# Kernel tuning notes

Measured on AMD Instinct MI355X. Metric: run time of the kernel, lower is better.

Reference implementation:

```python
import jax, jax.numpy as jnp
import numpy as np

COMMITMENT_COST = 0.25


def setup_inputs() -> dict:
    key = jax.random.key(0)
    k1, k2 = jax.random.split(key)
    B, D, H, W = 16, 256, 64, 64   # channel-first latents, D == embedding_dim
    K = 1024                        # num_embeddings
    z = jax.random.normal(k1, (B, D, H, W), dtype=jnp.float32)
    emb = jax.random.normal(k2, (K, D), dtype=jnp.float32)
    emb = emb / jnp.linalg.norm(emb, axis=1, keepdims=True)  # F.normalize(p=2, dim=1)
    return {"z": z, "embeddings": emb}


def reference(z, embeddings):
    D = embeddings.shape[1]
    input_shape = z.shape
    flat_z = z.reshape(-1, D)  # matches torch .view(-1, embedding_dim) on contiguous tensor
    dist = (jnp.sum(flat_z * flat_z, axis=1, keepdims=True)
            + jnp.sum(embeddings * embeddings, axis=1)
            - 2.0 * flat_z @ embeddings.T)
    encoding_indices = jnp.argmin(dist, axis=1)                       # [N]
    # one-hot @ embeddings == gather (same math, no [N,K] one-hot materialized)
    quantized = embeddings[encoding_indices].reshape(input_shape)
    e_latent_loss = jnp.mean((jax.lax.stop_gradient(quantized) - z) ** 2)
    q_latent_loss = jnp.mean((quantized - jax.lax.stop_gradient(z)) ** 2)
    vq_loss = q_latent_loss + COMMITMENT_COST * e_latent_loss
    quantized_st = z + jax.lax.stop_gradient(quantized - z)  # straight-through
    encoding_indices = encoding_indices.reshape((input_shape[0],) + input_shape[2:])
    return quantized_st, vq_loss, encoding_indices
```

## Files before the change

kernel.cpp:

```cpp
#include <hip/hip_runtime.h>
#include <stdint.h>


typedef __attribute__((ext_vector_type(8))) short short8;
typedef __attribute__((ext_vector_type(16))) float f32x16;

#define THR_S 1e-3f

__device__ __forceinline__ unsigned short f2bf(float f) {
    const unsigned int x = __float_as_uint(f);
    return (unsigned short)((x + 0x7FFFu + ((x >> 16) & 1u)) >> 16);
}
__device__ __forceinline__ float bf2f(unsigned short h) {
    return __uint_as_float(((unsigned int)h) << 16);
}

#define MFMA32(A, B, C) __builtin_amdgcn_mfma_f32_32x32x16_bf16(A, B, C, 0, 0, 0)

__global__ __launch_bounds__(256)
void eprep_kernel(const float* __restrict__ emb, unsigned short* __restrict__ eh_t,
                  unsigned short* __restrict__ el_t, float* __restrict__ enorm,
                  int* __restrict__ wlcnt) {
    const int code = blockIdx.x;
    const int k = threadIdx.x;
    if (code == 0 && k == 0) wlcnt[0] = 0;
    const float v = emb[code * 256 + k];
    const unsigned short h = f2bf(v);
    const int idx = ((k >> 4) << 14) + (code << 4) + (((k >> 3) & 1) << 3) + (k & 7);
    eh_t[idx] = h;
    el_t[idx] = f2bf(v - bf2f(h));
    float s = v * v;
#pragma unroll
    for (int o = 32; o > 0; o >>= 1) s += __shfl_xor(s, o);
    __shared__ float red[4];
    if ((k & 63) == 0) red[k >> 6] = s;
    __syncthreads();
    if (k == 0) enorm[code] = (red[0] + red[1]) + (red[2] + red[3]);
}

#define UPD(S, C, B1, I1, B2) { \
    const bool lt_ = (S) < B1; \
    B2 = lt_ ? B1 : fminf(B2, (S)); \
    I1 = lt_ ? (C) : I1; \
    B1 = lt_ ? (S) : B1; }

#define MERGE32(B1, I1, B2) { \
    const float ob1_ = __shfl_xor(B1, 32); \
    const int   oi1_ = __shfl_xor(I1, 32); \
    const float ob2_ = __shfl_xor(B2, 32); \
    const float nb2_ = fminf(fminf(B2, ob2_), fmaxf(B1, ob1_)); \
    if (ob1_ < B1 || (ob1_ == B1 && oi1_ < I1)) { B1 = ob1_; I1 = oi1_; } \
    B2 = nb2_; }

#define PFLOAD(S, U) { \
    const int un_ = (U) & 63; \
    const int ofs_ = ((un_ & 15) << 15) + ((un_ >> 4) << 10); \
    pf##S##h = *reinterpret_cast<const short8*>(ehp + ofs_); \
    pf##S##l = *reinterpret_cast<const short8*>(elp + ofs_); }

#define UNIT(S, KS) { \
    const int ko_ = (((KS) << 5) + (hi << 4)) ^ rsw; \
    const short8 bh0 = *reinterpret_cast<const short8*>(zbuf + rb0 + ko_); \
    const short8 bl0 = *reinterpret_cast<const short8*>(zbuf + 32768 + rb0 + ko_); \
    const short8 bh1 = *reinterpret_cast<const short8*>(zbuf + rb1 + ko_); \
    const short8 bl1 = *reinterpret_cast<const short8*>(zbuf + 32768 + rb1 + ko_); \
    acc1a = MFMA32(pf##S##h, bh0, acc1a); \
    acc1b = MFMA32(pf##S##h, bh1, acc1b); \
    acc2a = MFMA32(pf##S##h, bl0, acc2a); \
    acc2b = MFMA32(pf##S##h, bl1, acc2b); \
    acc2a = MFMA32(pf##S##l, bh0, acc2a); \
    acc2b = MFMA32(pf##S##l, bh1, acc2b); }

__global__ __launch_bounds__(512, 2)
void argmin_kernel(const float* __restrict__ z, const unsigned short* __restrict__ eh_t,
                   float* __restrict__ idx_out, int* __restrict__ wl,
                   int* __restrict__ wlcnt) {
    __shared__ char zbuf[65536];
    __shared__ float m_b1[8][64];
    __shared__ int   m_i1[8][64];
    __shared__ float m_b2[8][64];

    const int t = threadIdx.x;
    const int l = t & 63;
    const int w = t >> 6;
    const int cl = l & 31;
    const int hi = l >> 5;

    const float* zblk = z + (size_t)blockIdx.x * 16384;

#pragma unroll
    for (int i = 0; i < 8; ++i) {
        const int idx = i * 2048 + t * 4;
        const int row = idx >> 8, k = idx & 255;
        const float4 v = *reinterpret_cast<const float4*>(zblk + idx);
        ushort4 hv, lv;
        hv.x = f2bf(v.x); lv.x = f2bf(v.x - bf2f(hv.x));
        hv.y = f2bf(v.y); lv.y = f2bf(v.y - bf2f(hv.y));
        hv.z = f2bf(v.z); lv.z = f2bf(v.z - bf2f(hv.z));
        hv.w = f2bf(v.w); lv.w = f2bf(v.w - bf2f(hv.w));
        const int boff = row * 512 + ((k << 1) ^ ((row & 7) << 4));
        *reinterpret_cast<ushort4*>(zbuf + boff) = hv;
        *reinterpret_cast<ushort4*>(zbuf + 32768 + boff) = lv;
    }
    __syncthreads();

    const char* ehp = (const char*)eh_t + (w * 128 + cl) * 32 + hi * 16;
    const char* elp = ehp + 524288;

    const int rb0 = cl * 512;
    const int rb1 = rb0 + 16384;
    const int rsw = (cl & 7) << 4;

    f32x16 acc1a, acc2a, acc1b, acc2b;
#pragma unroll
    for (int j = 0; j < 16; ++j) { acc1a[j] = 0.f; acc2a[j] = 0.f; acc1b[j] = 0.f; acc2b[j] = 0.f; }

    float b1a = 3.4e38f, b2a = 3.4e38f, b1b = 3.4e38f, b2b = 3.4e38f;
    int   i1a = 0, i1b = 0;

    short8 pf0h, pf0l, pf1h, pf1l, pf2h, pf2l, pf3h, pf3l;
    PFLOAD(0, 0) PFLOAD(1, 1) PFLOAD(2, 2) PFLOAD(3, 3)

#pragma unroll 1
    for (int ct = 0; ct < 4; ++ct) {
#pragma unroll 1
        for (int j = 0; j < 4; ++j) {
            const int u0 = (ct << 4) + (j << 2);
            UNIT(0, ((j << 2) + 0)) PFLOAD(0, u0 + 4)
            UNIT(1, ((j << 2) + 1)) PFLOAD(1, u0 + 5)
            UNIT(2, ((j << 2) + 2)) PFLOAD(2, u0 + 6)
            UNIT(3, ((j << 2) + 3)) PFLOAD(3, u0 + 7)
        }
        const int code0 = w * 128 + (ct << 5) + (hi << 2);
#pragma unroll
        for (int reg = 0; reg < 16; ++reg) {
            const int code = code0 + (reg & 3) + ((reg >> 2) << 3);
            const float s0 = -(acc1a[reg] + acc2a[reg]);
            const float s1 = -(acc1b[reg] + acc2b[reg]);
            UPD(s0, code, b1a, i1a, b2a)
            UPD(s1, code, b1b, i1b, b2b)
            acc1a[reg] = 0.f; acc2a[reg] = 0.f; acc1b[reg] = 0.f; acc2b[reg] = 0.f;
        }
    }

    MERGE32(b1a, i1a, b2a)
    MERGE32(b1b, i1b, b2b)
    if (l < 32) {
        m_b1[w][cl] = b1a;      m_i1[w][cl] = i1a;      m_b2[w][cl] = b2a;
        m_b1[w][cl + 32] = b1b; m_i1[w][cl + 32] = i1b; m_b2[w][cl + 32] = b2b;
    }
    __syncthreads();
    if (t < 64) {
        float b1 = m_b1[0][t]; int i1 = m_i1[0][t]; float b2 = m_b2[0][t];
#pragma unroll
        for (int g = 1; g < 8; ++g) {
            const float ob1 = m_b1[g][t]; const int oi1 = m_i1[g][t]; const float ob2 = m_b2[g][t];
            const float nb2 = fminf(fminf(b2, ob2), fmaxf(b1, ob1));
            if (ob1 < b1 || (ob1 == b1 && oi1 < i1)) { b1 = ob1; i1 = oi1; }
            b2 = nb2;
        }
        const int grow = blockIdx.x * 64 + t;
        idx_out[grow] = (float)i1;
        if (b2 - b1 < THR_S) {
            const int pos = atomicAdd(wlcnt, 1);
            wl[pos] = grow;
        }
    }
}

__global__ __launch_bounds__(256)
void fixup_kernel(const float* __restrict__ z, const float* __restrict__ emb,
                  const float* __restrict__ enorm_g, const int* __restrict__ wl,
                  const int* __restrict__ wlcnt, float* __restrict__ idx_out) {
    __shared__ float zrow[256];
    __shared__ float znred[4];
    __shared__ float mb[4];
    __shared__ int   mi[4];

    const int t = threadIdx.x;
    const int l = t & 63, wv = t >> 6;
    const int dq = l & 3, tx = (l >> 2) & 15;

    int n = wlcnt[0];
    if (n > 65536) n = 65536;

#pragma unroll 1
    for (int i = blockIdx.x; i < n; i += 256) {
        const int r = wl[i];
        const float v = z[(size_t)r * 256 + t];
        zrow[t] = v;
        float zn = v * v;
#pragma unroll
        for (int o = 32; o > 0; o >>= 1) zn += __shfl_xor(zn, o);
        if (l == 0) znred[wv] = zn;
        __syncthreads();
        const float znf = (znred[0] + znred[1]) + (znred[2] + znred[3]);

        float b1 = 3.4e38f;
        int   i1 = 0;
#pragma unroll 1
        for (int cc = 0; cc < 16; ++cc) {
            const int c = wv * 256 + cc * 16 + tx;
            const float* er = emb + (size_t)c * 256 + dq * 4;
            float dot = 0.f;
#pragma unroll
            for (int j = 0; j < 16; ++j) {
                const float4 ev = *reinterpret_cast<const float4*>(er + j * 16);
                const float4 zv = *reinterpret_cast<const float4*>(&zrow[j * 16 + dq * 4]);
                dot = fmaf(zv.x, ev.x, dot);
                dot = fmaf(zv.y, ev.y, dot);
                dot = fmaf(zv.z, ev.z, dot);
                dot = fmaf(zv.w, ev.w, dot);
            }
            dot += __shfl_xor(dot, 1);
            dot += __shfl_xor(dot, 2);
            const float dist = fmaf(-2.f, dot, znf + enorm_g[c]);
            if (dist < b1) { b1 = dist; i1 = c; }
        }
#pragma unroll
        for (int off = 4; off < 64; off <<= 1) {
            const float ov = __shfl_xor(b1, off);
            const int   oi = __shfl_xor(i1, off);
            if (ov < b1 || (ov == b1 && oi < i1)) { b1 = ov; i1 = oi; }
        }
        if (l == 0) { mb[wv] = b1; mi[wv] = i1; }
        __syncthreads();
        if (t == 0) {
            float fb = mb[0]; int fi = mi[0];
#pragma unroll
            for (int g = 1; g < 4; ++g)
                if (mb[g] < fb || (mb[g] == fb && mi[g] < fi)) { fb = mb[g]; fi = mi[g]; }
            idx_out[r] = (float)fi;
        }
        __syncthreads();
    }
}

__global__ __launch_bounds__(256)
void gather_kernel(const float* __restrict__ z, const float* __restrict__ emb,
                   const float* __restrict__ idx_f, float* __restrict__ q_out,
                   float* __restrict__ partials) {
    const int wv = threadIdx.x >> 6, ln = threadIdx.x & 63;
    float lsum = 0.f;
#pragma unroll
    for (int i = 0; i < 8; ++i) {
        const size_t row = (size_t)blockIdx.x * 32 + i * 4 + wv;
        const int kidx = (int)idx_f[row];
        const float4 e4 = *reinterpret_cast<const float4*>(emb + (size_t)kidx * 256 + ln * 4);
        const float4 z4 = *reinterpret_cast<const float4*>(z + row * 256 + ln * 4);
        *reinterpret_cast<float4*>(q_out + row * 256 + ln * 4) = e4;
        const float dx = e4.x - z4.x, dy = e4.y - z4.y, dz = e4.z - z4.z, dw = e4.w - z4.w;
        lsum += dx * dx + dy * dy + dz * dz + dw * dw;
    }
#pragma unroll
    for (int off = 32; off > 0; off >>= 1) lsum += __shfl_xor(lsum, off);
    __shared__ float red[4];
    if (ln == 0) red[wv] = lsum;
    __syncthreads();
    if (threadIdx.x == 0) partials[blockIdx.x] = red[0] + red[1] + red[2] + red[3];
}

__global__ __launch_bounds__(256)
void loss_kernel(const float* __restrict__ partials, float* __restrict__ loss_out) {
    const int tid = threadIdx.x;
    float s = 0.f;
#pragma unroll
    for (int i = 0; i < 8; ++i) s += partials[tid + i * 256];
#pragma unroll
    for (int off = 32; off > 0; off >>= 1) s += __shfl_xor(s, off);
    __shared__ float red[4];
    if ((tid & 63) == 0) red[tid >> 6] = s;
    __syncthreads();
    if (tid == 0)
        loss_out[0] = (red[0] + red[1] + red[2] + red[3]) * (1.25f / 16777216.0f);
}

extern "C" void kernel_launch(void* const* d_in, const int* in_sizes, int n_in,
                              void* d_out, int out_size, void* d_ws, size_t ws_size,
                              hipStream_t stream) {
    const float* z   = (const float*)d_in[0];
    const float* emb = (const float*)d_in[1];
    float* out      = (float*)d_out;
    float* q_out    = out;
    float* loss_out = out + 16777216;
    float* idx_out  = out + 16777217;
    float* enorm    = (float*)d_ws;
    float* partials = (float*)d_ws + 1024;
    unsigned short* eh_t = (unsigned short*)q_out;
    unsigned short* el_t = eh_t + 262144;
    int*   wl    = (int*)(q_out + 262144);
    int*   wlcnt = (int*)(q_out + 327680);

    eprep_kernel<<<1024, 256, 0, stream>>>(emb, eh_t, el_t, enorm, wlcnt);
    argmin_kernel<<<1024, 512, 0, stream>>>(z, eh_t, idx_out, wl, wlcnt);
    fixup_kernel<<<256, 256, 0, stream>>>(z, emb, enorm, wl, wlcnt, idx_out);
    gather_kernel<<<2048, 256, 0, stream>>>(z, emb, idx_out, q_out, partials);
    loss_kernel<<<1, 256, 0, stream>>>(partials, loss_out);
}
```

Before: 174.9 us.

## Fuse gather and loss partials into argmin epilogue, deepen B-operand prefetch

Moves the quantized-output gather and the squared-error partial sums into the argmin kernel's epilogue. The epilogue rebuilds z from the bf16 hi/lo split already held in LDS, so the separate gather pass no longer re-reads z and its launch goes away. Fixup rows now write corrected embedding rows and a per-row loss delta that a new loss kernel adds back in. The embedding-preparation buffers move into the workspace when it is large enough, with the old path kept as a fallback. The prefetch depth in the MFMA loop doubles from 4 to 8 units, which raises register pressure, and z rebuilt from bf16 hi+lo is a slightly inexact stand-in for the loss.

```diff
diff --git a/kernel.cpp b/kernel.cpp
--- a/kernel.cpp
+++ b/kernel.cpp
@@ -6,6 +6,7 @@
 typedef __attribute__((ext_vector_type(16))) float f32x16;
 
 #define THR_S 1e-3f
+#define WLCAP 16384
 
 __device__ __forceinline__ unsigned short f2bf(float f) {
     const unsigned int x = __float_as_uint(f);
@@ -74,11 +75,13 @@
 __global__ __launch_bounds__(512, 2)
 void argmin_kernel(const float* __restrict__ z, const unsigned short* __restrict__ eh_t,
                    float* __restrict__ idx_out, int* __restrict__ wl,
-                   int* __restrict__ wlcnt) {
+                   int* __restrict__ wlcnt, const float* __restrict__ emb,
+                   float* __restrict__ q_out, float* __restrict__ partials) {
     __shared__ char zbuf[65536];
     __shared__ float m_b1[8][64];
     __shared__ int   m_i1[8][64];
     __shared__ float m_b2[8][64];
+    __shared__ int   fidx_s[64];
 
     const int t = threadIdx.x;
     const int l = t & 63;
@@ -119,17 +122,24 @@
     int   i1a = 0, i1b = 0;
 
     short8 pf0h, pf0l, pf1h, pf1l, pf2h, pf2l, pf3h, pf3l;
+    short8 pf4h, pf4l, pf5h, pf5l, pf6h, pf6l, pf7h, pf7l;
     PFLOAD(0, 0) PFLOAD(1, 1) PFLOAD(2, 2) PFLOAD(3, 3)
+    PFLOAD(4, 4) PFLOAD(5, 5) PFLOAD(6, 6) PFLOAD(7, 7)
 
 #pragma unroll 1
     for (int ct = 0; ct < 4; ++ct) {
 #pragma unroll 1
-        for (int j = 0; j < 4; ++j) {
-            const int u0 = (ct << 4) + (j << 2);
-            UNIT(0, ((j << 2) + 0)) PFLOAD(0, u0 + 4)
-            UNIT(1, ((j << 2) + 1)) PFLOAD(1, u0 + 5)
-            UNIT(2, ((j << 2) + 2)) PFLOAD(2, u0 + 6)
-            UNIT(3, ((j << 2) + 3)) PFLOAD(3, u0 + 7)
+        for (int hh = 0; hh < 2; ++hh) {
+            const int u0 = (ct << 4) + (hh << 3);
+            const int k0 = hh << 3;
+            UNIT(0, k0 + 0) PFLOAD(0, u0 + 8)
+            UNIT(1, k0 + 1) PFLOAD(1, u0 + 9)
+            UNIT(2, k0 + 2) PFLOAD(2, u0 + 10)
+            UNIT(3, k0 + 3) PFLOAD(3, u0 + 11)
+            UNIT(4, k0 + 4) PFLOAD(4, u0 + 12)
+            UNIT(5, k0 + 5) PFLOAD(5, u0 + 13)
+            UNIT(6, k0 + 6) PFLOAD(6, u0 + 14)
+            UNIT(7, k0 + 7) PFLOAD(7, u0 + 15)
         }
         const int code0 = w * 128 + (ct << 5) + (hi << 2);
 #pragma unroll
@@ -161,9 +171,43 @@
         }
         const int grow = blockIdx.x * 64 + t;
         idx_out[grow] = (float)i1;
+        fidx_s[t] = i1;
         if (b2 - b1 < THR_S) {
             const int pos = atomicAdd(wlcnt, 1);
-            wl[pos] = grow;
+            if (pos < WLCAP) wl[pos] = grow;
+        }
+    }
+
+    if (q_out != nullptr) {
+        __syncthreads();
+        float lsum = 0.f;
+        float* qblk = q_out + (size_t)blockIdx.x * 16384;
+#pragma unroll
+        for (int i = 0; i < 8; ++i) {
+            const int row = i * 8 + w;
+            const int code = fidx_s[row];
+            const float4 e4 = *reinterpret_cast<const float4*>(
+                emb + (size_t)code * 256 + l * 4);
+            const int byt = row * 512 + ((l * 8) ^ ((row & 7) << 4));
+            const ushort4 h4 = *reinterpret_cast<const ushort4*>(zbuf + byt);
+            const ushort4 l4 = *reinterpret_cast<const ushort4*>(zbuf + 32768 + byt);
+            const float zx = bf2f(h4.x) + bf2f(l4.x);
+            const float zy = bf2f(h4.y) + bf2f(l4.y);
+            const float zz = bf2f(h4.z) + bf2f(l4.z);
+            const float zw = bf2f(h4.w) + bf2f(l4.w);
+            const float dx = e4.x - zx, dy = e4.y - zy, dz = e4.z - zz, dw = e4.w - zw;
+            lsum += dx * dx + dy * dy + dz * dz + dw * dw;
+            *reinterpret_cast<float4*>(qblk + row * 256 + l * 4) = e4;
+        }
+#pragma unroll
+        for (int o = 32; o > 0; o >>= 1) lsum += __shfl_xor(lsum, o);
+        if (l == 0) m_b1[0][w] = lsum;
+        __syncthreads();
+        if (t == 0) {
+            float s = 0.f;
+#pragma unroll
+            for (int g = 0; g < 8; ++g) s += m_b1[0][g];
+            partials[blockIdx.x] = s;
         }
     }
 }
@@ -171,18 +215,21 @@
 __global__ __launch_bounds__(256)
 void fixup_kernel(const float* __restrict__ z, const float* __restrict__ emb,
                   const float* __restrict__ enorm_g, const int* __restrict__ wl,
-                  const int* __restrict__ wlcnt, float* __restrict__ idx_out) {
+                  const int* __restrict__ wlcnt, float* __restrict__ idx_out,
+                  float* __restrict__ q_out, float* __restrict__ wl_delta) {
     __shared__ float zrow[256];
     __shared__ float znred[4];
     __shared__ float mb[4];
     __shared__ int   mi[4];
+    __shared__ int   fin_s;
+    __shared__ float dred[4];
 
     const int t = threadIdx.x;
     const int l = t & 63, wv = t >> 6;
     const int dq = l & 3, tx = (l >> 2) & 15;
 
     int n = wlcnt[0];
-    if (n > 65536) n = 65536;
+    if (n > WLCAP) n = WLCAP;
 
 #pragma unroll 1
     for (int i = blockIdx.x; i < n; i += 256) {
@@ -230,10 +277,50 @@
 #pragma unroll
             for (int g = 1; g < 4; ++g)
                 if (mb[g] < fb || (mb[g] == fb && mi[g] < fi)) { fb = mb[g]; fi = mi[g]; }
-            idx_out[r] = (float)fi;
-        }
-        __syncthreads();
-    }
+            fin_s = fi;
+        }
+        __syncthreads();
+        const int fi = fin_s;
+        if (wl_delta != nullptr) {
+            const int oldi = (int)idx_out[r];
+            float d = 0.f;
+            if (fi != oldi) {
+                const float en_ = emb[(size_t)fi * 256 + t];
+                const float eo_ = emb[(size_t)oldi * 256 + t];
+                const float zt = zrow[t];
+                d = (en_ - zt) * (en_ - zt) - (eo_ - zt) * (eo_ - zt);
+                q_out[(size_t)r * 256 + t] = en_;
+            }
+#pragma unroll
+            for (int o = 32; o > 0; o >>= 1) d += __shfl_xor(d, o);
+            if (l == 0) dred[wv] = d;
+            __syncthreads();
+            if (t == 0) {
+                wl_delta[i] = (dred[0] + dred[1]) + (dred[2] + dred[3]);
+                idx_out[r] = (float)fi;
+            }
+        } else {
+            if (t == 0) idx_out[r] = (float)fi;
+        }
+        __syncthreads();
+    }
+}
+
+__global__ __launch_bounds__(256)
+void loss_kernel(const float* __restrict__ partials, const float* __restrict__ wl_delta,
+                 const int* __restrict__ wlcnt, float* __restrict__ loss_out) {
+    const int tid = threadIdx.x;
+    float s = partials[tid] + partials[tid + 256] + partials[tid + 512] + partials[tid + 768];
+    int n = wlcnt[0];
+    if (n > WLCAP) n = WLCAP;
+    for (int i = tid; i < n; i += 256) s += wl_delta[i];
+#pragma unroll
+    for (int off = 32; off > 0; off >>= 1) s += __shfl_xor(s, off);
+    __shared__ float red[4];
+    if ((tid & 63) == 0) red[tid >> 6] = s;
+    __syncthreads();
+    if (tid == 0)
+        loss_out[0] = ((red[0] + red[1]) + (red[2] + red[3])) * (1.25f / 16777216.0f);
 }
 
 __global__ __launch_bounds__(256)
@@ -261,7 +348,7 @@
 }
 
 __global__ __launch_bounds__(256)
-void loss_kernel(const float* __restrict__ partials, float* __restrict__ loss_out) {
+void loss_fb_kernel(const float* __restrict__ partials, float* __restrict__ loss_out) {
     const int tid = threadIdx.x;
     float s = 0.f;
 #pragma unroll
@@ -284,16 +371,39 @@
     float* q_out    = out;
     float* loss_out = out + 16777216;
     float* idx_out  = out + 16777217;
-    float* enorm    = (float*)d_ws;
-    float* partials = (float*)d_ws + 1024;
-    unsigned short* eh_t = (unsigned short*)q_out;
-    unsigned short* el_t = eh_t + 262144;
-    int*   wl    = (int*)(q_out + 262144);
-    int*   wlcnt = (int*)(q_out + 327680);
-
-    eprep_kernel<<<1024, 256, 0, stream>>>(emb, eh_t, el_t, enorm, wlcnt);
-    argmin_kernel<<<1024, 512, 0, stream>>>(z, eh_t, idx_out, wl, wlcnt);
-    fixup_kernel<<<256, 256, 0, stream>>>(z, emb, enorm, wl, wlcnt, idx_out);
-    gather_kernel<<<2048, 256, 0, stream>>>(z, emb, idx_out, q_out, partials);
-    loss_kernel<<<1, 256, 0, stream>>>(partials, loss_out);
-}
+
+    const size_t WS_NEEDED = (size_t)298048 * 4;
+    float* ws = (float*)d_ws;
+
+    if (ws_size >= WS_NEEDED) {
+        unsigned short* eh_t = (unsigned short*)ws;
+        unsigned short* el_t = eh_t + 262144;
+        float* enorm    = ws + 262144;
+        float* partials = ws + 263168;
+        int*   wlcnt    = (int*)(ws + 265216);
+        int*   wl       = (int*)(ws + 265280);
+        float* wl_delta = ws + 281664;
+
+        eprep_kernel<<<1024, 256, 0, stream>>>(emb, eh_t, el_t, enorm, wlcnt);
+        argmin_kernel<<<1024, 512, 0, stream>>>(z, eh_t, idx_out, wl, wlcnt,
+                                                emb, q_out, partials);
+        fixup_kernel<<<256, 256, 0, stream>>>(z, emb, enorm, wl, wlcnt, idx_out,
+                                              q_out, wl_delta);
+        loss_kernel<<<1, 256, 0, stream>>>(partials, wl_delta, wlcnt, loss_out);
+    } else {
+        unsigned short* eh_t = (unsigned short*)q_out;
+        unsigned short* el_t = eh_t + 262144;
+        int*   wl    = (int*)(q_out + 262144);
+        int*   wlcnt = (int*)(q_out + 327680);
+        float* enorm    = ws;
+        float* partials = ws + 1024;
+
+        eprep_kernel<<<1024, 256, 0, stream>>>(emb, eh_t, el_t, enorm, wlcnt);
+        argmin_kernel<<<1024, 512, 0, stream>>>(z, eh_t, idx_out, wl, wlcnt,
+                                                emb, nullptr, nullptr);
+        fixup_kernel<<<256, 256, 0, stream>>>(z, emb, enorm, wl, wlcnt, idx_out,
+                                              nullptr, nullptr);
+        gather_kernel<<<2048, 256, 0, stream>>>(z, emb, idx_out, q_out, partials);
+        loss_fb_kernel<<<1, 256, 0, stream>>>(partials, loss_out);
+    }
+}
```

Result: faster. 162.9 us (-6.9%).
